# Kernel optimization log

Measured on AMD Instinct MI355X. Metric: run time of the kernel, lower is better.

## Reference

```python
import jax, jax.numpy as jnp
import numpy as np

B, S, D, H, L, FF, HID, OUT = 64, 255, 512, 8, 6, 2048, 256, 1
DK = D // H
EPS = 1e-5


def layer_norm(x, g, b):
    m = jnp.mean(x, axis=-1, keepdims=True)
    v = jnp.mean((x - m) ** 2, axis=-1, keepdims=True)
    return (x - m) * jax.lax.rsqrt(v + EPS) * g + b


def setup_inputs() -> dict:
    key = jax.random.key(0)
    ks = jax.random.split(key, 32)
    atom_emb = jax.random.normal(ks[0], (B, S, D), dtype=jnp.float32)
    edge_bias = jax.random.normal(ks[1], (B, S, S, H), dtype=jnp.float32) * 0.1
    lengths = jax.random.randint(ks[2], (B,), S // 2, S + 1)
    key_padding_mask = jnp.arange(S)[None, :] >= lengths[:, None]  # True = pad
    sd = 1.0 / np.sqrt(D)
    sf = 1.0 / np.sqrt(FF)
    return {
        "atom_emb": atom_emb,
        "edge_bias": edge_bias,
        "key_padding_mask": key_padding_mask,
        "cls_token": jax.random.normal(ks[3], (1, 1, D), dtype=jnp.float32),
        "Wq": jax.random.normal(ks[4], (L, D, D), dtype=jnp.float32) * sd,
        "bq": jnp.zeros((L, D), jnp.float32),
        "Wk": jax.random.normal(ks[5], (L, D, D), dtype=jnp.float32) * sd,
        "bk": jnp.zeros((L, D), jnp.float32),
        "Wv": jax.random.normal(ks[6], (L, D, D), dtype=jnp.float32) * sd,
        "bv": jnp.zeros((L, D), jnp.float32),
        "Wo": jax.random.normal(ks[7], (L, D, D), dtype=jnp.float32) * sd,
        "bo": jnp.zeros((L, D), jnp.float32),
        "ln1_g": jnp.ones((L, D), jnp.float32),
        "ln1_b": jnp.zeros((L, D), jnp.float32),
        "W1": jax.random.normal(ks[8], (L, D, FF), dtype=jnp.float32) * sd,
        "b1": jnp.zeros((L, FF), jnp.float32),
        "W2": jax.random.normal(ks[9], (L, FF, D), dtype=jnp.float32) * sf,
        "b2": jnp.zeros((L, D), jnp.float32),
        "ln2_g": jnp.ones((L, D), jnp.float32),
        "ln2_b": jnp.zeros((L, D), jnp.float32),
        "head_W1": jax.random.normal(ks[10], (D, HID), dtype=jnp.float32) * sd,
        "head_b1": jnp.zeros((HID,), jnp.float32),
        "head_W2": jax.random.normal(ks[11], (HID, OUT), dtype=jnp.float32) / np.sqrt(HID),
        "head_b2": jnp.zeros((OUT,), jnp.float32),
    }


def reference(atom_emb, edge_bias, key_padding_mask, cls_token, Wq, bq, Wk, bk, Wv, bv,
              Wo, bo, ln1_g, ln1_b, W1, b1, W2, b2, ln2_g, ln2_b,
              head_W1, head_b1, head_W2, head_b2):
    b = atom_emb.shape[0]
    # CLS pooling: prepend learned token -> seq len S+1
    x = jnp.concatenate([jnp.broadcast_to(cls_token, (b, 1, D)), atom_emb], axis=1)
    # expand edge bias with zero row/col for CLS, move heads to axis 1
    bias_h = jnp.pad(edge_bias, ((0, 0), (1, 0), (1, 0), (0, 0))).transpose(0, 3, 1, 2)
    mask = jnp.concatenate([jnp.zeros((b, 1), bool), key_padding_mask], axis=1)  # [B,S+1]
    neg = jnp.finfo(jnp.float32).min
    scale = 1.0 / np.sqrt(DK)
    sp1 = x.shape[1]
    for l in range(L):
        q = (x @ Wq[l] + bq[l]).reshape(b, sp1, H, DK)
        k = (x @ Wk[l] + bk[l]).reshape(b, sp1, H, DK)
        v = (x @ Wv[l] + bv[l]).reshape(b, sp1, H, DK)
        scores = jnp.einsum('bihd,bjhd->bhij', q, k) * scale + bias_h
        scores = jnp.where(mask[:, None, None, :], neg, scores)
        attn = jax.nn.softmax(scores, axis=-1)
        out = jnp.einsum('bhij,bjhd->bihd', attn, v).reshape(b, sp1, D)
        out = out @ Wo[l] + bo[l]
        x = layer_norm(x + out, ln1_g[l], ln1_b[l])
        ff = jax.nn.gelu(x @ W1[l] + b1[l], approximate=False) @ W2[l] + b2[l]
        x = layer_norm(x + ff, ln2_g[l], ln2_b[l])
    cls = x[:, 0]  # [B, D]
    h = jax.nn.gelu(cls @ head_W1 + head_b1, approximate=False)
    return h @ head_W2 + head_b2  # [B, 1]
```

## Files before the change

### kernel.cpp

```cpp
#include <hip/hip_runtime.h>
#include <math.h>
#include <stdint.h>

#define B_   64
#define S_   255
#define SP   256
#define D_   512
#define H_   8
#define L_   6
#define FF_  2048
#define HID_ 256
#define N_   (B_*SP)
#define EPS  1e-5f

using bf16x8 = __bf16 __attribute__((ext_vector_type(8)));
using f32x4  = float __attribute__((ext_vector_type(4)));
using u16x4  = unsigned short __attribute__((ext_vector_type(4)));

__device__ inline float wave_sum(float v) {
#pragma unroll
    for (int off = 32; off; off >>= 1) v += __shfl_xor(v, off);
    return v;
}

__device__ inline float gelu_exact(float x) {
    float z  = fabsf(x) * 0.70710678118654752f;
    float tt = __builtin_amdgcn_rcpf(fmaf(0.3275911f, z, 1.0f));
    float poly = tt * (0.254829592f + tt * (-0.284496736f + tt * (1.421413741f +
                 tt * (-1.453152027f + tt * 1.061405429f))));
    float er = 1.0f - poly * __expf(-z * z);
    er = copysignf(er, x);
    return 0.5f * x * (1.0f + er);
}

__device__ inline unsigned short bf_bits(float x) {
    __bf16 h = (__bf16)x;
    return *(unsigned short*)&h;
}

__device__ inline float bf_val(unsigned short u) {
    __bf16 h = *(__bf16*)&u;
    return (float)h;
}

__device__ inline uint8_t enc_e4m3(float f) {
    uint32_t u = __float_as_uint(f);
    uint32_t s = (u >> 24) & 0x80u;
    float a = fabsf(f);
    if (a < 0.015625f) {
        int m = (int)rintf(a * 512.0f);
        if (m >= 8) return (uint8_t)(s | 0x08);
        return (uint8_t)(s | (uint32_t)m);
    }
    if (a > 448.0f) return (uint8_t)(s | 0x7E);
    uint32_t b = __float_as_uint(a);
    uint32_t expf_ = b >> 23;
    uint32_t mant = b & 0x7FFFFF;
    uint32_t keep = mant >> 20;
    uint32_t rest = mant & 0xFFFFF;
    if (rest > 0x80000u || (rest == 0x80000u && (keep & 1))) keep++;
    if (keep == 8) { keep = 0; expf_++; }
    int e8 = (int)expf_ - 120;
    if (e8 >= 16) return (uint8_t)(s | 0x7E);
    return (uint8_t)(s | ((uint32_t)e8 << 3) | keep);
}

__device__ inline float dec_e4m3(uint32_t b) {
    uint32_t mag = b & 0x7Fu;
    float fm = __uint_as_float((mag << 20) + (120u << 23));
    if ((mag >> 3) == 0) fm = fm * 2.0f - 0.015625f;
    return (b & 0x80u) ? -fm : fm;
}

#define GLOAD16(gsrc, ldst) \
    __builtin_amdgcn_global_load_lds((const __attribute__((address_space(1))) unsigned int*)(gsrc), \
                                     (__attribute__((address_space(3))) unsigned int*)(ldst), 16, 0, 0)

__global__ void k_build_x(const float* __restrict__ atom, const float* __restrict__ cls,
                          __bf16* __restrict__ Xb) {
    int idx = blockIdx.x * 256 + threadIdx.x;
    int col = idx & (D_ - 1);
    int row = idx >> 9;
    int sr  = row & (SP - 1);
    int b   = row >> 8;
    float v = (sr == 0) ? cls[col] : atom[((size_t)(b * S_) + (sr - 1)) * D_ + col];
    Xb[idx] = (__bf16)v;
}

__global__ void k_mask_detect(const unsigned int* __restrict__ mw, int nw, int* flag) {
    int i = blockIdx.x * 256 + threadIdx.x;
    if (i < nw && mw[i] > 1u) atomicOr(flag, 1);
}

__global__ void k_mask_prep(const void* __restrict__ mraw, const int* __restrict__ flag,
                            float* __restrict__ mskadd) {
    int i = blockIdx.x * 256 + threadIdx.x;
    int b = i >> 8, j = i & 255;
    float v = 0.0f;
    if (j > 0) {
        int src = b * S_ + (j - 1);
        bool m = (*flag) ? (((const unsigned char*)mraw)[src] != 0)
                         : (((const int*)mraw)[src] != 0);
        if (m) v = -1e30f;
    }
    mskadd[i] = v;
}

__global__ __launch_bounds__(256) void k_wt(const float* __restrict__ W, __bf16* __restrict__ Wt,
                                            int K, int Mw, int mout_off,
                                            size_t in_lstride, size_t out_lstride) {
    __shared__ float T[64][65];
    int l = blockIdx.z;
    int m0 = blockIdx.x * 64, k0 = blockIdx.y * 64;
    const float* Wl = W + (size_t)l * in_lstride;
    __bf16* Wtl = Wt + (size_t)l * out_lstride;
    int tid = threadIdx.x;
    int cc = tid & 63, rr = tid >> 6;
#pragma unroll
    for (int p = 0; p < 16; p++) {
        int kk = rr + p * 4;
        T[kk][cc] = Wl[(size_t)(k0 + kk) * Mw + m0 + cc];
    }
    __syncthreads();
#pragma unroll
    for (int p = 0; p < 16; p++) {
        int mm = rr + p * 4;
        Wtl[(size_t)(mout_off + m0 + mm) * K + k0 + cc] = (__bf16)T[cc][mm];
    }
}

__global__ void k_bcat(const float* __restrict__ bq, const float* __restrict__ bk,
                       const float* __restrict__ bv, float* __restrict__ bqkv) {
    int i = blockIdx.x * 256 + threadIdx.x;
    int l = i / 1536, c = i % 1536;
    float v;
    if (c < 512)       v = bq[l * 512 + c];
    else if (c < 1024) v = bk[l * 512 + c - 512];
    else               v = bv[l * 512 + c - 1024];
    bqkv[i] = v;
}

__global__ __launch_bounds__(256) void k_ebt5(const float* __restrict__ eb, uint8_t* __restrict__ ebt) {
    __shared__ uint8_t Ls[8 * 16 * 260];
    int blk = blockIdx.x;
    int b = blk >> 4, wm = blk & 15;
    int w = wm >> 2, mq = wm & 3;
    int qbase = w * 64 + mq * 16;
    int t = threadIdx.x;
    for (int qi = 0; qi < 16; qi++) {
        int q = qbase + qi;
        if (q > 0) {
            const float4* src = (const float4*)(eb + ((size_t)(b * 255) + (q - 1)) * 2040);
#pragma unroll
            for (int p = 0; p < 2; p++) {
                int idx4 = t + p * 256;
                if (idx4 < 510) {
                    float4 v = src[idx4];
                    int k  = idx4 >> 1;
                    int h0 = (idx4 & 1) * 4;
                    Ls[((h0 + 0) * 16 + qi) * 260 + k] = enc_e4m3(v.x);
                    Ls[((h0 + 1) * 16 + qi) * 260 + k] = enc_e4m3(v.y);
                    Ls[((h0 + 2) * 16 + qi) * 260 + k] = enc_e4m3(v.z);
                    Ls[((h0 + 3) * 16 + qi) * 260 + k] = enc_e4m3(v.w);
                }
            }
        }
    }
    __syncthreads();
    int cc = t >> 4, qi = t & 15;
    int q = qbase + qi;
    uint32_t* outp = (uint32_t*)ebt;
#pragma unroll
    for (int h = 0; h < 8; h++) {
#pragma unroll
        for (int tl = 0; tl < 4; tl++) {
            uint32_t d = 0;
            if (q > 0) {
#pragma unroll
                for (int nk = 0; nk < 4; nk++) {
                    int k = tl * 64 + nk * 16 + cc;
                    if (k > 0) d |= (uint32_t)Ls[(h * 16 + qi) * 260 + (k - 1)] << (nk * 8);
                }
            }
            size_t x = ((((size_t)(b * 8 + h) * 4 + tl) * 4 + w) * 4 + mq) * 256 + t;
            outp[x] = d;
        }
    }
}

template<int GELU>
__global__ __launch_bounds__(512, 2) void k_gemm2(const __bf16* __restrict__ Ag,
                                                  const __bf16* __restrict__ Bg,
                                                  const float* __restrict__ bias,
                                                  __bf16* __restrict__ Cb,
                                                  __bf16* __restrict__ vtout,
                                                  int K, int M, int gx) {
    __shared__ __align__(16) __bf16 AS[128 * 64];
    __shared__ __align__(16) __bf16 BS[128 * 64];
    const int tid = threadIdx.x;
    const int w = tid >> 6, lane = tid & 63;
    const int wr = w >> 2, wc = w & 3;
    const int lrow = lane & 15, lg = lane >> 4;
    const int nwg = gridDim.x, bid = blockIdx.x;
    const int swz = (bid & 7) * (nwg >> 3) + (bid >> 3);
    const int by = swz / gx, bx = swz - by * gx;
    const int rowbase = by * 128, colbase = bx * 128;
    const int nkt = K >> 6;

    f32x4 acc[4][2];
#pragma unroll
    for (int m = 0; m < 4; m++)
#pragma unroll
        for (int n = 0; n < 2; n++) acc[m][n] = f32x4{0.f, 0.f, 0.f, 0.f};

    for (int kt = 0; kt < nkt; ++kt) {
        if (kt) __builtin_amdgcn_s_barrier();
        __builtin_amdgcn_sched_barrier(0);
#pragma unroll
        for (int p = 0; p < 2; p++) {
            int s = tid + p * 512;
            int row = s >> 3, sg = s & 7;
            GLOAD16(Ag + (size_t)(rowbase + row) * K + kt * 64 + ((sg ^ (row & 7)) << 3), &AS[s * 8]);
            GLOAD16(Bg + (size_t)(colbase + row) * K + kt * 64 + ((sg ^ (row & 7)) << 3), &BS[s * 8]);
        }
        asm volatile("s_waitcnt vmcnt(0)" ::: "memory");
        __builtin_amdgcn_s_barrier();

        bf16x8 aF[4][2], bF[2][2];
#pragma unroll
        for (int m = 0; m < 4; m++) {
            int arow = wr * 64 + m * 16 + lrow;
#pragma unroll
            for (int ks = 0; ks < 2; ks++) {
                int sl = (lg + ks * 4) ^ (arow & 7);
                aF[m][ks] = *(const bf16x8*)&AS[arow * 64 + sl * 8];
            }
        }
#pragma unroll
        for (int n = 0; n < 2; n++) {
            int brow = wc * 32 + n * 16 + lrow;
#pragma unroll
            for (int ks = 0; ks < 2; ks++) {
                int sl = (lg + ks * 4) ^ (brow & 7);
                bF[n][ks] = *(const bf16x8*)&BS[brow * 64 + sl * 8];
            }
        }
        asm volatile("s_waitcnt lgkmcnt(0)" ::: "memory");
        __builtin_amdgcn_sched_barrier(0);
        __builtin_amdgcn_s_setprio(1);
#pragma unroll
        for (int m = 0; m < 4; m++)
#pragma unroll
            for (int n = 0; n < 2; n++)
#pragma unroll
                for (int ks = 0; ks < 2; ks++)
                    acc[m][n] = __builtin_amdgcn_mfma_f32_16x16x32_bf16(aF[m][ks], bF[n][ks],
                                                                        acc[m][n], 0, 0, 0);
        __builtin_amdgcn_s_setprio(0);
    }

    const bool dovt = (vtout != nullptr) && (colbase >= 1024);
#pragma unroll
    for (int m = 0; m < 4; m++) {
        int row = rowbase + wr * 64 + m * 16 + lg * 4;
#pragma unroll
        for (int n = 0; n < 2; n++) {
            int col = colbase + wc * 32 + n * 16 + lrow;
            float bv = bias ? bias[col] : 0.0f;
            float v[4];
#pragma unroll
            for (int r = 0; r < 4; r++) {
                float x = acc[m][n][r] + bv;
                if (GELU) x = gelu_exact(x);
                v[r] = x;
            }
            if (dovt) {
                int hcol = col - 1024;
                int hh = hcol >> 6, d = hcol & 63;
                int bb = row >> 8, s0 = row & 255;
                u16x4 pk = { bf_bits(v[0]), bf_bits(v[1]), bf_bits(v[2]), bf_bits(v[3]) };
                *(u16x4*)&vtout[((size_t)((bb * 8 + hh) * 64 + d)) * 256 + s0] = pk;
            } else {
#pragma unroll
                for (int r = 0; r < 4; r++)
                    Cb[(size_t)(row + r) * M + col] = (__bf16)v[r];
            }
        }
    }
}

__global__ __launch_bounds__(256) void k_attn(const __bf16* __restrict__ QKV,
                                              const uint8_t* __restrict__ ebt,
                                              const float* __restrict__ mskadd,
                                              const __bf16* __restrict__ Vt,
                                              __bf16* __restrict__ T) {
    __shared__ __align__(16) char Ks[8192];
    __shared__ __align__(16) char Vs[8192];
    __shared__ __align__(16) char Ps[4][2048];
    __shared__ float Ma[256];
    const int bid = blockIdx.x;
    const int swzb = (bid & 7) * 256 + (bid >> 3);
    const int bh = swzb >> 2, qt = swzb & 3;
    const int b = bh >> 3, h = bh & 7;
    const int tid = threadIdx.x, wid = tid >> 6, lane = tid & 63;
    const int g = lane >> 4, c = lane & 15;

    Ma[tid] = mskadd[(b << 8) + tid];

    bf16x8 qf[2];
    {
        const __bf16* qrow = QKV + (size_t)((b << 8) + qt * 64 + wid * 16 + c) * 1536 + h * 64;
        qf[0] = *(const bf16x8*)(qrow + g * 8);
        qf[1] = *(const bf16x8*)(qrow + 32 + g * 8);
    }

    f32x4 oacc[4];
    float m_s[4], l_s[4];
#pragma unroll
    for (int r = 0; r < 4; r++) { m_s[r] = -1e30f; l_s[r] = 0.0f; }
#pragma unroll
    for (int nd = 0; nd < 4; nd++) oacc[nd] = f32x4{0.f, 0.f, 0.f, 0.f};

    for (int t = 0; t < 4; t++) {
        const int t0 = t * 64;
        __syncthreads();
        if (t0 > 0 && Ma[t0] < -0.5f) continue;
#pragma unroll
        for (int p = 0; p < 2; p++) {
            int idx = tid + p * 256;
            int row = idx >> 3, c8 = idx & 7;
            int lds = row * 128 + ((c8 * 16) ^ ((row & 7) << 4));
            *(uint4*)(Ks + lds) = *(const uint4*)&QKV[(size_t)((b << 8) + t0 + row) * 1536 + 512 + h * 64 + c8 * 8];
            *(uint4*)(Vs + lds) = *(const uint4*)&Vt[((size_t)bh * 64 + row) * 256 + t0 + c8 * 8];
        }
        __syncthreads();

        bf16x8 kf[4][2], vb[4][2];
#pragma unroll
        for (int n = 0; n < 4; n++) {
            int row = n * 16 + c;
#pragma unroll
            for (int ks = 0; ks < 2; ks++) {
                int col = (g * 16 + ks * 64) ^ ((row & 7) << 4);
                kf[n][ks] = *(const bf16x8*)(Ks + row * 128 + col);
                vb[n][ks] = *(const bf16x8*)(Vs + row * 128 + col);
            }
        }

        f32x4 sa[4];
#pragma unroll
        for (int nk = 0; nk < 4; nk++) sa[nk] = f32x4{0.f, 0.f, 0.f, 0.f};
#pragma unroll
        for (int ks = 0; ks < 2; ks++)
#pragma unroll
            for (int nk = 0; nk < 4; nk++)
                sa[nk] = __builtin_amdgcn_mfma_f32_16x16x32_bf16(qf[ks], kf[nk][ks], sa[nk], 0, 0, 0);

        uint4 b4 = *(const uint4*)(ebt + ((((size_t)bh * 4 + t) * 4 + qt) * 4 + wid) * 1024 + c * 64 + g * 16);
        uint32_t bw[4] = { b4.x, b4.y, b4.z, b4.w };
        float s[4][4];
#pragma unroll
        for (int nk = 0; nk < 4; nk++) {
            float ma = Ma[t0 + nk * 16 + c];
#pragma unroll
            for (int r = 0; r < 4; r++)
                s[nk][r] = sa[nk][r] * 0.125f + dec_e4m3((bw[r] >> (nk * 8)) & 0xFF) + ma;
        }

        float corr[4];
#pragma unroll
        for (int r = 0; r < 4; r++) {
            float tm = fmaxf(fmaxf(s[0][r], s[1][r]), fmaxf(s[2][r], s[3][r]));
#pragma unroll
            for (int off = 1; off < 16; off <<= 1)
                tm = fmaxf(tm, __shfl_xor(tm, off));
            float mnew = fmaxf(m_s[r], tm);
            corr[r] = __expf(m_s[r] - mnew);
            m_s[r] = mnew;
            float psum = 0.0f;
#pragma unroll
            for (int nk = 0; nk < 4; nk++) {
                s[nk][r] = __expf(s[nk][r] - mnew);
                psum += s[nk][r];
            }
#pragma unroll
            for (int off = 1; off < 16; off <<= 1)
                psum += __shfl_xor(psum, off);
            l_s[r] = l_s[r] * corr[r] + psum;
        }
#pragma unroll
        for (int nd = 0; nd < 4; nd++)
#pragma unroll
            for (int r = 0; r < 4; r++)
                oacc[nd][r] *= corr[r];

        char* psw = Ps[wid];
#pragma unroll
        for (int r = 0; r < 4; r++) {
            int qs = g * 4 + r;
#pragma unroll
            for (int nk = 0; nk < 4; nk++)
                *(__bf16*)(psw + qs * 128 + ((nk * 32 + c * 2) ^ ((qs & 7) << 4))) = (__bf16)s[nk][r];
        }
        bf16x8 pa[2];
#pragma unroll
        for (int ks = 0; ks < 2; ks++)
            pa[ks] = *(const bf16x8*)(psw + c * 128 + ((g * 16 + ks * 64) ^ ((c & 7) << 4)));
#pragma unroll
        for (int nd = 0; nd < 4; nd++)
#pragma unroll
            for (int ks = 0; ks < 2; ks++)
                oacc[nd] = __builtin_amdgcn_mfma_f32_16x16x32_bf16(pa[ks], vb[nd][ks], oacc[nd], 0, 0, 0);
    }

#pragma unroll
    for (int r = 0; r < 4; r++) {
        float inv = 1.0f / l_s[r];
        size_t rowb = (size_t)((b << 8) + qt * 64 + wid * 16 + g * 4 + r) * 512 + h * 64 + c;
#pragma unroll
        for (int nd = 0; nd < 4; nd++)
            T[rowb + nd * 16] = (__bf16)(oacc[nd][r] * inv);
    }
}

__global__ __launch_bounds__(256) void k_ln3(const __bf16* __restrict__ Ob,
                                             __bf16* __restrict__ Xb,
                                             const float* __restrict__ g,
                                             const float* __restrict__ bb) {
    __shared__ float red[4];
    int row = blockIdx.x, t = threadIdx.x;
    size_t base = (size_t)row * D_;
    uint ov = *(const uint*)&Ob[base + 2 * t];
    uint xv = *(const uint*)&Xb[base + 2 * t];
    float v0 = bf_val((unsigned short)xv) + bf_val((unsigned short)ov);
    float v1 = bf_val((unsigned short)(xv >> 16)) + bf_val((unsigned short)(ov >> 16));
    float s = wave_sum(v0 + v1);
    if ((t & 63) == 0) red[t >> 6] = s;
    __syncthreads();
    float mean = (red[0] + red[1] + red[2] + red[3]) * (1.0f / D_);
    float d0 = v0 - mean, d1 = v1 - mean;
    float s2 = wave_sum(d0 * d0 + d1 * d1);
    __syncthreads();
    if ((t & 63) == 0) red[t >> 6] = s2;
    __syncthreads();
    float var = (red[0] + red[1] + red[2] + red[3]) * (1.0f / D_);
    float rr = rsqrtf(var + EPS);
    float2 gv = *(const float2*)&g[2 * t];
    float2 bv = *(const float2*)&bb[2 * t];
    float o0 = d0 * rr * gv.x + bv.x;
    float o1 = d1 * rr * gv.y + bv.y;
    uint pk = (uint)bf_bits(o0) | ((uint)bf_bits(o1) << 16);
    *(uint*)&Xb[base + 2 * t] = pk;
}

__global__ __launch_bounds__(256) void k_head(const __bf16* __restrict__ Xb,
                                              const float* __restrict__ W1,
                                              const float* __restrict__ b1,
                                              const float* __restrict__ W2,
                                              const float* __restrict__ b2,
                                              float* __restrict__ out) {
    __shared__ float cls[D_];
    __shared__ float red[4];
    int b = blockIdx.x, t = threadIdx.x;
    size_t base = (size_t)(b << 8) * D_;
    cls[t]       = (float)Xb[base + t];
    cls[t + 256] = (float)Xb[base + t + 256];
    __syncthreads();
    float acc = 0.0f;
    for (int d = 0; d < D_; d++) acc = fmaf(cls[d], W1[(size_t)d * HID_ + t], acc);
    acc += b1[t];
    float hsum = wave_sum(gelu_exact(acc) * W2[t]);
    if ((t & 63) == 0) red[t >> 6] = hsum;
    __syncthreads();
    if (t == 0) out[b] = red[0] + red[1] + red[2] + red[3] + b2[0];
}

extern "C" void kernel_launch(void* const* d_in, const int* in_sizes, int n_in,
                              void* d_out, int out_size, void* d_ws, size_t ws_size,
                              hipStream_t stream) {
    const float* atom = (const float*)d_in[0];
    const float* eb   = (const float*)d_in[1];
    const void*  mraw = d_in[2];
    const float* cls  = (const float*)d_in[3];
    const float* Wq = (const float*)d_in[4];  const float* bq = (const float*)d_in[5];
    const float* Wk = (const float*)d_in[6];  const float* bk = (const float*)d_in[7];
    const float* Wv = (const float*)d_in[8];  const float* bv = (const float*)d_in[9];
    const float* Wo = (const float*)d_in[10]; const float* bo = (const float*)d_in[11];
    const float* g1 = (const float*)d_in[12]; const float* be1 = (const float*)d_in[13];
    const float* W1 = (const float*)d_in[14]; const float* b1 = (const float*)d_in[15];
    const float* W2 = (const float*)d_in[16]; const float* b2 = (const float*)d_in[17];
    const float* g2 = (const float*)d_in[18]; const float* be2 = (const float*)d_in[19];
    const float* hW1 = (const float*)d_in[20]; const float* hb1 = (const float*)d_in[21];
    const float* hW2 = (const float*)d_in[22]; const float* hb2 = (const float*)d_in[23];
    float* out = (float*)d_out;

    char* p = (char*)d_ws;
    __bf16* Xb    = (__bf16*)p;                p += (size_t)N_ * D_ * 2;
    __bf16* Vt    = (__bf16*)p;                p += (size_t)N_ * D_ * 2;
    __bf16* Ob    = (__bf16*)p;                p += (size_t)N_ * D_ * 2;
    char*   R     = p;                         p += (size_t)N_ * FF_ * 2;
    __bf16* QKVb  = (__bf16*)R;
    __bf16* Tb    = (__bf16*)(R + (size_t)N_ * 1536 * 2);
    __bf16* Hb    = (__bf16*)R;
    uint8_t* ebt  = (uint8_t*)p;               p += (size_t)B_ * H_ * SP * SP;
    __bf16* Wqkvt = (__bf16*)p;                p += (size_t)L_ * 1536 * 512 * 2;
    __bf16* Wot   = (__bf16*)p;                p += (size_t)L_ * 512 * 512 * 2;
    __bf16* W1t   = (__bf16*)p;                p += (size_t)L_ * 2048 * 512 * 2;
    __bf16* W2t   = (__bf16*)p;                p += (size_t)L_ * 512 * 2048 * 2;
    float*  bqkv  = (float*)p;                 p += (size_t)L_ * 1536 * 4;
    float*  mskadd= (float*)p;                 p += (size_t)B_ * SP * 4;
    int* flag = (int*)p;

    hipMemsetAsync(flag, 0, 4, stream);
    k_mask_detect<<<16, 256, 0, stream>>>((const unsigned int*)mraw, (B_ * S_) / 4, flag);
    k_mask_prep<<<(B_ * SP) / 256, 256, 0, stream>>>(mraw, flag, mskadd);
    k_bcat<<<(L_ * 1536) / 256, 256, 0, stream>>>(bq, bk, bv, bqkv);
    k_wt<<<dim3(8, 8, L_),  256, 0, stream>>>(Wq, Wqkvt, 512, 512, 0,    262144, 786432);
    k_wt<<<dim3(8, 8, L_),  256, 0, stream>>>(Wk, Wqkvt, 512, 512, 512,  262144, 786432);
    k_wt<<<dim3(8, 8, L_),  256, 0, stream>>>(Wv, Wqkvt, 512, 512, 1024, 262144, 786432);
    k_wt<<<dim3(8, 8, L_),  256, 0, stream>>>(Wo, Wot,   512, 512, 0,    262144, 262144);
    k_wt<<<dim3(32, 8, L_), 256, 0, stream>>>(W1, W1t,   512, 2048, 0,   1048576, 1048576);
    k_wt<<<dim3(8, 32, L_), 256, 0, stream>>>(W2, W2t,   2048, 512, 0,   1048576, 1048576);
    k_ebt5<<<B_ * 16, 256, 0, stream>>>(eb, ebt);
    k_build_x<<<(N_ * D_) / 256, 256, 0, stream>>>(atom, cls, Xb);

    for (int l = 0; l < L_; l++) {
        k_gemm2<0><<<1536, 512, 0, stream>>>(Xb, Wqkvt + (size_t)l * 786432, bqkv + l * 1536,
                                             QKVb, Vt, 512, 1536, 12);
        k_attn<<<B_ * H_ * 4, 256, 0, stream>>>(QKVb, ebt, mskadd, Vt, Tb);
        k_gemm2<0><<<512, 512, 0, stream>>>(Tb, Wot + (size_t)l * 262144, bo + l * 512,
                                            Ob, nullptr, 512, 512, 4);
        k_ln3<<<N_, 256, 0, stream>>>(Ob, Xb, g1 + l * D_, be1 + l * D_);
        k_gemm2<1><<<2048, 512, 0, stream>>>(Xb, W1t + (size_t)l * 1048576, b1 + l * FF_,
                                             Hb, nullptr, 512, 2048, 16);
        k_gemm2<0><<<512, 512, 0, stream>>>(Hb, W2t + (size_t)l * 1048576, b2 + l * D_,
                                            Ob, nullptr, 2048, 512, 4);
        k_ln3<<<N_, 256, 0, stream>>>(Ob, Xb, g2 + l * D_, be2 + l * D_);
    }
    k_head<<<B_, 256, 0, stream>>>(Xb, hW1, hb1, hW2, hb2, out);
}
```

Measured before the change: 1.466 ms.

## Double-buffer LDS tiles in GEMM to overlap global loads with MFMA

Splits the A and B shared-memory tiles of the GEMM kernel into two buffers. The next k-tile is now issued with async global-to-LDS loads before the current tile is read and multiplied, so load latency can hide behind MFMA work instead of stalling every iteration. The cost is twice the LDS per block (64KB), which may limit the two-blocks-per-CU occupancy requested in launch bounds.

New measurement: 1.443 ms. About the same (-1.6%).

```diff
diff --git a/kernel.cpp b/kernel.cpp
--- a/kernel.cpp
+++ b/kernel.cpp
@@ -195,8 +195,8 @@
                                                   __bf16* __restrict__ Cb,
                                                   __bf16* __restrict__ vtout,
                                                   int K, int M, int gx) {
-    __shared__ __align__(16) __bf16 AS[128 * 64];
-    __shared__ __align__(16) __bf16 BS[128 * 64];
+    __shared__ __align__(16) __bf16 AS[2][128 * 64];
+    __shared__ __align__(16) __bf16 BS[2][128 * 64];
     const int tid = threadIdx.x;
     const int w = tid >> 6, lane = tid & 63;
     const int wr = w >> 2, wc = w & 3;
@@ -207,24 +207,32 @@
     const int rowbase = by * 128, colbase = bx * 128;
     const int nkt = K >> 6;
 
+#define STAGE(buf_, kt_) do {                                                              \
+        _Pragma("unroll")                                                                  \
+        for (int p_ = 0; p_ < 2; p_++) {                                                   \
+            int s_ = tid + p_ * 512;                                                       \
+            int row_ = s_ >> 3, sg_ = s_ & 7;                                              \
+            GLOAD16(Ag + (size_t)(rowbase + row_) * K + (kt_) * 64 + ((sg_ ^ (row_ & 7)) << 3), \
+                    &AS[buf_][s_ * 8]);                                                    \
+            GLOAD16(Bg + (size_t)(colbase + row_) * K + (kt_) * 64 + ((sg_ ^ (row_ & 7)) << 3), \
+                    &BS[buf_][s_ * 8]);                                                    \
+        }                                                                                  \
+    } while (0)
+
     f32x4 acc[4][2];
 #pragma unroll
     for (int m = 0; m < 4; m++)
 #pragma unroll
         for (int n = 0; n < 2; n++) acc[m][n] = f32x4{0.f, 0.f, 0.f, 0.f};
 
+    STAGE(0, 0);
+    asm volatile("s_waitcnt vmcnt(0)" ::: "memory");
+    __builtin_amdgcn_s_barrier();
+
     for (int kt = 0; kt < nkt; ++kt) {
-        if (kt) __builtin_amdgcn_s_barrier();
+        const int cur = kt & 1;
+        if (kt + 1 < nkt) STAGE(cur ^ 1, kt + 1);
         __builtin_amdgcn_sched_barrier(0);
-#pragma unroll
-        for (int p = 0; p < 2; p++) {
-            int s = tid + p * 512;
-            int row = s >> 3, sg = s & 7;
-            GLOAD16(Ag + (size_t)(rowbase + row) * K + kt * 64 + ((sg ^ (row & 7)) << 3), &AS[s * 8]);
-            GLOAD16(Bg + (size_t)(colbase + row) * K + kt * 64 + ((sg ^ (row & 7)) << 3), &BS[s * 8]);
-        }
-        asm volatile("s_waitcnt vmcnt(0)" ::: "memory");
-        __builtin_amdgcn_s_barrier();
 
         bf16x8 aF[4][2], bF[2][2];
 #pragma unroll
@@ -233,7 +241,7 @@
 #pragma unroll
             for (int ks = 0; ks < 2; ks++) {
                 int sl = (lg + ks * 4) ^ (arow & 7);
-                aF[m][ks] = *(const bf16x8*)&AS[arow * 64 + sl * 8];
+                aF[m][ks] = *(const bf16x8*)&AS[cur][arow * 64 + sl * 8];
             }
         }
 #pragma unroll
@@ -242,7 +250,7 @@
 #pragma unroll
             for (int ks = 0; ks < 2; ks++) {
                 int sl = (lg + ks * 4) ^ (brow & 7);
-                bF[n][ks] = *(const bf16x8*)&BS[brow * 64 + sl * 8];
+                bF[n][ks] = *(const bf16x8*)&BS[cur][brow * 64 + sl * 8];
             }
         }
         asm volatile("s_waitcnt lgkmcnt(0)" ::: "memory");
@@ -257,7 +265,10 @@
                     acc[m][n] = __builtin_amdgcn_mfma_f32_16x16x32_bf16(aF[m][ks], bF[n][ks],
                                                                         acc[m][n], 0, 0, 0);
         __builtin_amdgcn_s_setprio(0);
-    }
+        asm volatile("s_waitcnt vmcnt(0)" ::: "memory");
+        __builtin_amdgcn_s_barrier();
+    }
+#undef STAGE
 
     const bool dovt = (vtout != nullptr) && (colbase >= 1024);
 #pragma unroll
```
